# Optimization experiments

Hardware: AMD Instinct MI355X
Metric: run time of the kernel (lower is better)

The kernel has to match this reference:

```python
import jax, jax.numpy as jnp
import numpy as np

B, S, D, H = 4, 1024, 1024, 16
HD = D // H  # head dim = 64


def setup_inputs() -> dict:
    key = jax.random.key(0)
    ks = jax.random.split(key, 12)
    inv = 1.0 / np.sqrt(D)
    inp = {
        "q": jax.random.normal(ks[0], (B, S, D), jnp.float32),
        "k": jax.random.normal(ks[1], (B, S, D), jnp.float32),
        "v": jax.random.normal(ks[2], (B, S, D), jnp.float32),
        # additive-style mask: 1 where attention is disallowed (causal)
        "mask": jnp.triu(jnp.ones((S, S), jnp.float32), k=1)[None, None, :, :],
        "Wq": jax.random.normal(ks[3], (D, D), jnp.float32) * inv,
        "bq": jnp.zeros((D,), jnp.float32),
        "Wk": jax.random.normal(ks[4], (D, D), jnp.float32) * inv,
        "bk": jnp.zeros((D,), jnp.float32),
        "Wv": jax.random.normal(ks[5], (D, D), jnp.float32) * inv,
        "bv": jnp.zeros((D,), jnp.float32),
        "Wo": jax.random.normal(ks[6], (D, D), jnp.float32) * inv,
        "bo": jnp.zeros((D,), jnp.float32),
    }
    return inp


def _split_heads(x):
    # [b, s, (h d)] -> [b, h, s, d]
    b, s, _ = x.shape
    return x.reshape(b, s, H, HD).transpose(0, 2, 1, 3)


def reference(q, k, v, mask, Wq, bq, Wk, bk, Wv, bv, Wo, bo):
    query = _split_heads(q @ Wq + bq)   # [b,h,s,d]
    key = _split_heads(k @ Wk + bk)
    value = _split_heads(v @ Wv + bv)

    scores = jnp.einsum("bhqd,bhkd->bhqk", query, key) / np.sqrt(HD)
    scores = scores + mask * (-1e12)
    attention_weights = jax.nn.softmax(scores, axis=-1)  # [b,h,s,s]
    attn = jnp.einsum("bhqk,bhkd->bhqd", attention_weights, value)

    # dropout is identity in eval mode
    attn = attn.transpose(0, 2, 1, 3).reshape(q.shape[0], q.shape[1], D)
    out = attn @ Wo + bo
    return out, attention_weights
```

## Files before the change

kernel.cpp:

```cpp
#include <hip/hip_runtime.h>
#include <hip/hip_bf16.h>

#define B_ 4
#define S_ 1024
#define D_ 1024
#define H_ 16
#define HD_ 64
#define M_ (B_*S_)
#define NT_ (S_/64)

typedef __attribute__((ext_vector_type(8))) short bf16x8;
typedef __attribute__((ext_vector_type(8))) unsigned short u16x8;
typedef __attribute__((ext_vector_type(4))) float f32x4;

typedef __attribute__((address_space(1))) const unsigned int g_uint;
typedef __attribute__((address_space(3))) unsigned int l_uint;

__device__ __forceinline__ unsigned short f2bf(float f) {
  unsigned int x = __builtin_bit_cast(unsigned int, f);
  unsigned int r = (x + 0x7fffu + ((x >> 16) & 1u)) >> 16;
  return (unsigned short)r;
}
__device__ __forceinline__ float bf2f(unsigned short u) {
  unsigned int x = ((unsigned int)u) << 16;
  return __builtin_bit_cast(float, x);
}
__device__ __forceinline__ void load_lds16(const ushort* g, ushort* l) {
  __builtin_amdgcn_global_load_lds((g_uint*)g, (l_uint*)l, 16, 0, 0);
}

__global__ void cvt3(const float* __restrict__ q, const float* __restrict__ k,
                     const float* __restrict__ v, ushort* __restrict__ qo,
                     ushort* __restrict__ ko, ushort* __restrict__ vo) {
  const float* s; ushort* d;
  switch (blockIdx.y) {
    case 0: s = q; d = qo; break;
    case 1: s = k; d = ko; break;
    default: s = v; d = vo; break;
  }
  int n4 = (M_ * D_) / 4;
  for (int i = blockIdx.x * blockDim.x + threadIdx.x; i < n4; i += gridDim.x * blockDim.x) {
    float4 x = reinterpret_cast<const float4*>(s)[i];
    ushort4 o;
    o.x = f2bf(x.x); o.y = f2bf(x.y); o.z = f2bf(x.z); o.w = f2bf(x.w);
    reinterpret_cast<ushort4*>(d)[i] = o;
  }
}

__global__ void tr4(const float* __restrict__ Wq, const float* __restrict__ Wk,
                    const float* __restrict__ Wv, const float* __restrict__ Wo,
                    ushort* __restrict__ q, ushort* __restrict__ k,
                    ushort* __restrict__ v, ushort* __restrict__ o) {
  const float* W; ushort* WT;
  switch (blockIdx.z) {
    case 0: W = Wq; WT = q; break;
    case 1: W = Wk; WT = k; break;
    case 2: W = Wv; WT = v; break;
    default: W = Wo; WT = o; break;
  }
  __shared__ float tile[32][33];
  int tx = threadIdx.x & 31, ty = threadIdx.x >> 5;
  int bx = blockIdx.x * 32, by = blockIdx.y * 32;
  for (int r = 0; r < 32; r += 8)
    tile[ty + r][tx] = W[(size_t)(by + ty + r) * D_ + bx + tx];
  __syncthreads();
  for (int r = 0; r < 32; r += 8)
    WT[(size_t)(bx + ty + r) * D_ + by + tx] = f2bf(tile[tx][ty + r]);
}

template <int BF16OUT>
__device__ __forceinline__ void gemm_body(const ushort* __restrict__ A,
                                          const ushort* __restrict__ Bt,
                                          const float* __restrict__ bias,
                                          void* __restrict__ Cp,
                                          int bm, int bn, int N, int K) {
  __shared__ ushort Al[128 * 64];
  __shared__ ushort Bl[128 * 64];
  const int tid = threadIdx.x;
  const int wave = tid >> 6, lane = tid & 63;
  const int r0 = lane & 15, kq = lane >> 4;
  const int wr = wave >> 1, wc = wave & 1;
  const int sl = lane >> 3;
  const int sc8 = ((lane & 7) ^ sl) * 8;
  f32x4 zero = {0.f, 0.f, 0.f, 0.f};
  f32x4 acc[4][4];
#pragma unroll
  for (int m = 0; m < 4; ++m)
#pragma unroll
    for (int n = 0; n < 4; ++n) acc[m][n] = zero;

  for (int kt = 0; kt < K; kt += 64) {
    __syncthreads();
#pragma unroll
    for (int i = 0; i < 4; ++i) {
      int c = wave * 4 + i;
      load_lds16(A  + (size_t)(bm + c * 8 + sl) * K + kt + sc8, &Al[c * 512]);
      load_lds16(Bt + (size_t)(bn + c * 8 + sl) * K + kt + sc8, &Bl[c * 512]);
    }
    __syncthreads();
#pragma unroll
    for (int kk = 0; kk < 2; ++kk) {
      bf16x8 a[4], b[4];
#pragma unroll
      for (int m = 0; m < 4; ++m)
        a[m] = *(const bf16x8*)&Al[(wr * 64 + m * 16 + r0) * 64 + (((kk * 4 + kq) ^ (r0 & 7)) * 8)];
#pragma unroll
      for (int n = 0; n < 4; ++n)
        b[n] = *(const bf16x8*)&Bl[(wc * 64 + n * 16 + r0) * 64 + (((kk * 4 + kq) ^ (r0 & 7)) * 8)];
#pragma unroll
      for (int m = 0; m < 4; ++m)
#pragma unroll
        for (int n = 0; n < 4; ++n)
          acc[m][n] = __builtin_amdgcn_mfma_f32_16x16x32_bf16(a[m], b[n], acc[m][n], 0, 0, 0);
    }
  }

#pragma unroll
  for (int m = 0; m < 4; ++m) {
#pragma unroll
    for (int n = 0; n < 4; ++n) {
      int col = bn + wc * 64 + n * 16 + r0;
      float bv = bias[col];
#pragma unroll
      for (int j = 0; j < 4; ++j) {
        int row = bm + wr * 64 + m * 16 + kq * 4 + j;
        float v = acc[m][n][j] + bv;
        if (BF16OUT) ((ushort*)Cp)[(size_t)row * N + col] = f2bf(v);
        else         ((float*)Cp)[(size_t)row * N + col] = v;
      }
    }
  }
}

__global__ __launch_bounds__(256) void gemm_qkv(const ushort* __restrict__ qa,
                                                const ushort* __restrict__ ka,
                                                const ushort* __restrict__ va,
                                                const ushort* __restrict__ WqT,
                                                const ushort* __restrict__ WkT,
                                                const ushort* __restrict__ WvT,
                                                const float* __restrict__ bq,
                                                const float* __restrict__ bk,
                                                const float* __restrict__ bv,
                                                ushort* __restrict__ Qo,
                                                ushort* __restrict__ Ko,
                                                ushort* __restrict__ Vo) {
  const ushort* A; const ushort* Bt; const float* bias; ushort* C;
  switch (blockIdx.z) {
    case 0: A = qa; Bt = WqT; bias = bq; C = Qo; break;
    case 1: A = ka; Bt = WkT; bias = bk; C = Ko; break;
    default: A = va; Bt = WvT; bias = bv; C = Vo; break;
  }
  gemm_body<1>(A, Bt, bias, C, blockIdx.x * 128, blockIdx.y * 128, D_, D_);
}

__global__ __launch_bounds__(256) void gemm_out(const ushort* __restrict__ A,
                                                const ushort* __restrict__ Bt,
                                                const float* __restrict__ bias,
                                                float* __restrict__ C) {
  gemm_body<0>(A, Bt, bias, C, blockIdx.x * 128, blockIdx.y * 128, D_, D_);
}

__global__ __launch_bounds__(256) void attn_fused(const ushort* __restrict__ Qb,
                                                  const ushort* __restrict__ Kb,
                                                  const ushort* __restrict__ Vb,
                                                  float* __restrict__ wout,
                                                  ushort* __restrict__ ctx) {
  const int id = blockIdx.x;
  const int bh = id & 63;
  const int b = bh >> 4, h = bh & 15;
  const int qt = NT_ - 1 - (id >> 6);
  const int tid = threadIdx.x, wave = tid >> 6, lane = tid & 63;
  const int r0 = lane & 15, kq = lane >> 4;
  const int sl = lane >> 3;
  const int sc8 = ((lane & 7) ^ sl) * 8;
  __shared__ ushort Kt[2][64 * 64];
  __shared__ ushort Vt[2][64 * 64];
  __shared__ ushort Wl[4][16 * 64];
  __shared__ float rs_lds[4][16];
  const size_t bh_off = ((size_t)(b * S_)) * D_ + (size_t)h * 64;
  float* wbase = wout + (size_t)bh * S_ * S_;

  const ushort* Qg = Qb + bh_off + (size_t)(qt * 64 + wave * 16 + r0) * D_ + kq * 8;
  bf16x8 qa0 = *(const bf16x8*)Qg;
  bf16x8 qa1 = *(const bf16x8*)(Qg + 32);
  const int grow0 = qt * 64 + wave * 16 + kq * 4;

  auto stage_K = [&](int buf, int vb) {
    const ushort* Kg = Kb + bh_off + (size_t)(vb * 64) * D_;
#pragma unroll
    for (int i = 0; i < 2; ++i) {
      int c = wave * 2 + i;
      load_lds16(Kg + (size_t)(c * 8 + sl) * D_ + sc8, &Kt[buf][c * 512]);
    }
  };

  int cur = 0;
  stage_K(0, 0);
  float partial[4] = {0.f, 0.f, 0.f, 0.f};
  for (int vb = 0; vb <= qt; ++vb) {
    asm volatile("s_waitcnt vmcnt(0)" ::: "memory");
    __builtin_amdgcn_s_barrier();
    if (vb < qt) stage_K(cur ^ 1, vb + 1);
    const bool diag = (vb == qt);
#pragma unroll
    for (int jt = 0; jt < 4; ++jt) {
      int krow = jt * 16 + r0;
      bf16x8 kb0 = *(const bf16x8*)&Kt[cur][krow * 64 + ((kq ^ (r0 & 7)) * 8)];
      bf16x8 kb1 = *(const bf16x8*)&Kt[cur][krow * 64 + (((4 + kq) ^ (r0 & 7)) * 8)];
      f32x4 sc = {0.f, 0.f, 0.f, 0.f};
      sc = __builtin_amdgcn_mfma_f32_16x16x32_bf16(qa0, kb0, sc, 0, 0, 0);
      sc = __builtin_amdgcn_mfma_f32_16x16x32_bf16(qa1, kb1, sc, 0, 0, 0);
      int col = vb * 64 + krow;
#pragma unroll
      for (int j = 0; j < 4; ++j) {
        float e = (diag && col > grow0 + j) ? 0.f : __expf(sc[j] * 0.125f);
        partial[j] += e;
      }
    }
    cur ^= 1;
  }
  float rs[4];
#pragma unroll
  for (int j = 0; j < 4; ++j) {
    float s = partial[j];
#pragma unroll
    for (int off = 1; off < 16; off <<= 1) s += __shfl_xor(s, off, 64);
    rs[j] = 1.f / s;
  }
  if (r0 == 0) {
#pragma unroll
    for (int j = 0; j < 4; ++j) rs_lds[wave][kq * 4 + j] = rs[j];
  }

  f32x4 zero = {0.f, 0.f, 0.f, 0.f};
  f32x4 cacc[4];
#pragma unroll
  for (int nt = 0; nt < 4; ++nt) cacc[nt] = zero;

  __syncthreads();
  const int row16 = lane >> 2, c4 = lane & 3;
  const float sclw = rs_lds[wave][row16];
  uint4 vr[2];
  auto vload = [&](int vb) {
    const ushort* Vg = Vb + bh_off + (size_t)(vb * 64) * D_;
    vr[0] = *(const uint4*)&Vg[(size_t)lane * D_ + (size_t)(wave * 2 + 0) * 8];
    vr[1] = *(const uint4*)&Vg[(size_t)lane * D_ + (size_t)(wave * 2 + 1) * 8];
  };
  auto vwrite = [&](int buf) {
#pragma unroll
    for (int it = 0; it < 2; ++it) {
      int seg = wave * 2 + it;
      ushort tmp[8];
      *(uint4*)tmp = vr[it];
#pragma unroll
      for (int e = 0; e < 8; ++e) Vt[buf][(seg * 8 + e) * 64 + (lane ^ (e << 3))] = tmp[e];
    }
  };
  cur = 0;
  stage_K(0, 0);
  vload(0);
  vwrite(0);
  for (int vb = 0; vb <= qt; ++vb) {
    if (vb == 0) asm volatile("s_waitcnt vmcnt(0) lgkmcnt(0)" ::: "memory");
    else         asm volatile("s_waitcnt vmcnt(4) lgkmcnt(0)" ::: "memory");
    __builtin_amdgcn_s_barrier();
    if (vb < qt) { stage_K(cur ^ 1, vb + 1); vload(vb + 1); }
    const bool diag = (vb == qt);
#pragma unroll
    for (int jt = 0; jt < 4; ++jt) {
      int krow = jt * 16 + r0;
      bf16x8 kb0 = *(const bf16x8*)&Kt[cur][krow * 64 + ((kq ^ (r0 & 7)) * 8)];
      bf16x8 kb1 = *(const bf16x8*)&Kt[cur][krow * 64 + (((4 + kq) ^ (r0 & 7)) * 8)];
      f32x4 sc = {0.f, 0.f, 0.f, 0.f};
      sc = __builtin_amdgcn_mfma_f32_16x16x32_bf16(qa0, kb0, sc, 0, 0, 0);
      sc = __builtin_amdgcn_mfma_f32_16x16x32_bf16(qa1, kb1, sc, 0, 0, 0);
      int col = vb * 64 + krow;
#pragma unroll
      for (int j = 0; j < 4; ++j) {
        int rowW = kq * 4 + j;
        float e = (diag && col > grow0 + j) ? 0.f : __expf(sc[j] * 0.125f);
        Wl[wave][rowW * 64 + ((jt * 16 + r0) ^ ((rowW & 7) << 3))] = f2bf(e);
      }
    }
#pragma unroll
    for (int ks = 0; ks < 2; ++ks) {
      bf16x8 af = *(const bf16x8*)&Wl[wave][r0 * 64 + (((ks * 4 + kq) ^ (r0 & 7)) * 8)];
#pragma unroll
      for (int nt = 0; nt < 4; ++nt) {
        bf16x8 vf = *(const bf16x8*)&Vt[cur][(nt * 16 + r0) * 64 + (((ks * 4 + kq) ^ (r0 & 7)) * 8)];
        cacc[nt] = __builtin_amdgcn_mfma_f32_16x16x32_bf16(af, vf, cacc[nt], 0, 0, 0);
      }
    }
    {
      int slotA = (2 * c4) ^ (row16 & 7);
      int slotB = (2 * c4 + 1) ^ (row16 & 7);
      u16x8 w0 = *(const u16x8*)&Wl[wave][row16 * 64 + slotA * 8];
      u16x8 w1 = *(const u16x8*)&Wl[wave][row16 * 64 + slotB * 8];
      float* dst = &wbase[(size_t)(qt * 64 + wave * 16 + row16) * S_ + vb * 64 + c4 * 16];
      f32x4 o0 = {bf2f(w0[0]) * sclw, bf2f(w0[1]) * sclw, bf2f(w0[2]) * sclw, bf2f(w0[3]) * sclw};
      f32x4 o1 = {bf2f(w0[4]) * sclw, bf2f(w0[5]) * sclw, bf2f(w0[6]) * sclw, bf2f(w0[7]) * sclw};
      f32x4 o2 = {bf2f(w1[0]) * sclw, bf2f(w1[1]) * sclw, bf2f(w1[2]) * sclw, bf2f(w1[3]) * sclw};
      f32x4 o3 = {bf2f(w1[4]) * sclw, bf2f(w1[5]) * sclw, bf2f(w1[6]) * sclw, bf2f(w1[7]) * sclw};
      *(f32x4*)&dst[0]  = o0;
      *(f32x4*)&dst[4]  = o1;
      *(f32x4*)&dst[8]  = o2;
      *(f32x4*)&dst[12] = o3;
    }
    if (vb < qt) vwrite(cur ^ 1);
    cur ^= 1;
  }

  {
    int col0 = (qt + 1) * 64;
    int nf4 = (S_ - col0) >> 2;
    int row = tid >> 2, c = tid & 3;
    f32x4 z4 = {0.f, 0.f, 0.f, 0.f};
    float* rp = &wbase[(size_t)(qt * 64 + row) * S_];
    for (int i = c; i < nf4; i += 4) *(f32x4*)&rp[col0 + i * 4] = z4;
  }

  {
    ushort* cg = ctx + ((size_t)(b * S_ + qt * 64 + wave * 16 + kq * 4)) * D_ + h * 64;
#pragma unroll
    for (int nt = 0; nt < 4; ++nt)
#pragma unroll
      for (int j = 0; j < 4; ++j)
        cg[(size_t)j * D_ + nt * 16 + r0] = f2bf(cacc[nt][j] * rs[j]);
  }
}

extern "C" void kernel_launch(void* const* d_in, const int* in_sizes, int n_in,
                              void* d_out, int out_size, void* d_ws, size_t ws_size,
                              hipStream_t stream) {
  const float* q    = (const float*)d_in[0];
  const float* k    = (const float*)d_in[1];
  const float* v    = (const float*)d_in[2];
  const float* Wq   = (const float*)d_in[4];
  const float* bq   = (const float*)d_in[5];
  const float* Wk   = (const float*)d_in[6];
  const float* bk   = (const float*)d_in[7];
  const float* Wv   = (const float*)d_in[8];
  const float* bv   = (const float*)d_in[9];
  const float* Wo   = (const float*)d_in[10];
  const float* bo   = (const float*)d_in[11];

  char* ws = (char*)d_ws;
  const size_t MB = 1024 * 1024;
  ushort* q_bf   = (ushort*)(ws + 0 * MB);
  ushort* k_bf   = (ushort*)(ws + 8 * MB);
  ushort* v_bf   = (ushort*)(ws + 16 * MB);
  ushort* WqT    = (ushort*)(ws + 24 * MB);
  ushort* WkT    = (ushort*)(ws + 26 * MB);
  ushort* WvT    = (ushort*)(ws + 28 * MB);
  ushort* WoT    = (ushort*)(ws + 30 * MB);
  ushort* Q_bf   = (ushort*)(ws + 32 * MB);
  ushort* K_bf   = (ushort*)(ws + 40 * MB);
  ushort* V_bf   = (ushort*)(ws + 48 * MB);
  ushort* ctx_bf = (ushort*)(ws + 56 * MB);

  float* out  = (float*)d_out;
  float* wout = out + (size_t)M_ * D_;

  cvt3<<<dim3(2048, 3), 256, 0, stream>>>(q, k, v, q_bf, k_bf, v_bf);
  tr4<<<dim3(32, 32, 4), 256, 0, stream>>>(Wq, Wk, Wv, Wo, WqT, WkT, WvT, WoT);
  gemm_qkv<<<dim3(M_ / 128, D_ / 128, 3), 256, 0, stream>>>(
      q_bf, k_bf, v_bf, WqT, WkT, WvT, bq, bk, bv, Q_bf, K_bf, V_bf);
  attn_fused<<<dim3(1024), 256, 0, stream>>>(Q_bf, K_bf, V_bf, wout, ctx_bf);
  gemm_out<<<dim3(M_ / 128, D_ / 128), 256, 0, stream>>>(ctx_bf, WoT, bo, out);
}
```

Baseline: 169.5 us.

## Transpose QK^T MFMA so lanes own query rows and write weights directly

Swaps the MFMA operands so each lane holds four consecutive key columns for a single query row. Row sums then need only two cross-lane shuffles, and the normalized fp32 attention weights can be stored straight from registers as float4. This drops the LDS round-trip and the bf16-to-fp32 reconversion that the weight output path used before. It also replaces __expf with exp2f using a pre-folded log2e scale and packs the bf16 conversions with v_cvt_pk_bf16_f32 under a new LDS swizzle. In exchange, the global weight stores become 16-byte per-lane writes scattered across 16 rows, which may coalesce worse than the previous 64-byte row segments.

```diff
diff --git a/kernel.cpp b/kernel.cpp
--- a/kernel.cpp
+++ b/kernel.cpp
@@ -24,6 +24,11 @@
 __device__ __forceinline__ float bf2f(unsigned short u) {
   unsigned int x = ((unsigned int)u) << 16;
   return __builtin_bit_cast(float, x);
+}
+__device__ __forceinline__ unsigned int cvtpk(float lo, float hi) {
+  unsigned int r;
+  asm("v_cvt_pk_bf16_f32 %0, %1, %2" : "=v"(r) : "v"(lo), "v"(hi));
+  return r;
 }
 __device__ __forceinline__ void load_lds16(const ushort* g, ushort* l) {
   __builtin_amdgcn_global_load_lds((g_uint*)g, (l_uint*)l, 16, 0, 0);
@@ -176,14 +181,14 @@
   __shared__ ushort Kt[2][64 * 64];
   __shared__ ushort Vt[2][64 * 64];
   __shared__ ushort Wl[4][16 * 64];
-  __shared__ float rs_lds[4][16];
   const size_t bh_off = ((size_t)(b * S_)) * D_ + (size_t)h * 64;
   float* wbase = wout + (size_t)bh * S_ * S_;
+  const float KSC = 0.18033688011f;
 
   const ushort* Qg = Qb + bh_off + (size_t)(qt * 64 + wave * 16 + r0) * D_ + kq * 8;
   bf16x8 qa0 = *(const bf16x8*)Qg;
   bf16x8 qa1 = *(const bf16x8*)(Qg + 32);
-  const int grow0 = qt * 64 + wave * 16 + kq * 4;
+  const int qglob = qt * 64 + wave * 16 + r0;
 
   auto stage_K = [&](int buf, int vb) {
     const ushort* Kg = Kb + bh_off + (size_t)(vb * 64) * D_;
@@ -196,7 +201,7 @@
 
   int cur = 0;
   stage_K(0, 0);
-  float partial[4] = {0.f, 0.f, 0.f, 0.f};
+  float p0 = 0.f, p1 = 0.f, p2 = 0.f, p3 = 0.f;
   for (int vb = 0; vb <= qt; ++vb) {
     asm volatile("s_waitcnt vmcnt(0)" ::: "memory");
     __builtin_amdgcn_s_barrier();
@@ -208,29 +213,20 @@
       bf16x8 kb0 = *(const bf16x8*)&Kt[cur][krow * 64 + ((kq ^ (r0 & 7)) * 8)];
       bf16x8 kb1 = *(const bf16x8*)&Kt[cur][krow * 64 + (((4 + kq) ^ (r0 & 7)) * 8)];
       f32x4 sc = {0.f, 0.f, 0.f, 0.f};
-      sc = __builtin_amdgcn_mfma_f32_16x16x32_bf16(qa0, kb0, sc, 0, 0, 0);
-      sc = __builtin_amdgcn_mfma_f32_16x16x32_bf16(qa1, kb1, sc, 0, 0, 0);
-      int col = vb * 64 + krow;
-#pragma unroll
-      for (int j = 0; j < 4; ++j) {
-        float e = (diag && col > grow0 + j) ? 0.f : __expf(sc[j] * 0.125f);
-        partial[j] += e;
-      }
+      sc = __builtin_amdgcn_mfma_f32_16x16x32_bf16(kb0, qa0, sc, 0, 0, 0);
+      sc = __builtin_amdgcn_mfma_f32_16x16x32_bf16(kb1, qa1, sc, 0, 0, 0);
+      int k0 = vb * 64 + jt * 16 + kq * 4;
+      p0 += (diag && k0 + 0 > qglob) ? 0.f : exp2f(sc[0] * KSC);
+      p1 += (diag && k0 + 1 > qglob) ? 0.f : exp2f(sc[1] * KSC);
+      p2 += (diag && k0 + 2 > qglob) ? 0.f : exp2f(sc[2] * KSC);
+      p3 += (diag && k0 + 3 > qglob) ? 0.f : exp2f(sc[3] * KSC);
     }
     cur ^= 1;
   }
-  float rs[4];
-#pragma unroll
-  for (int j = 0; j < 4; ++j) {
-    float s = partial[j];
-#pragma unroll
-    for (int off = 1; off < 16; off <<= 1) s += __shfl_xor(s, off, 64);
-    rs[j] = 1.f / s;
-  }
-  if (r0 == 0) {
-#pragma unroll
-    for (int j = 0; j < 4; ++j) rs_lds[wave][kq * 4 + j] = rs[j];
-  }
+  float ssum = (p0 + p1) + (p2 + p3);
+  ssum += __shfl_xor(ssum, 16, 64);
+  ssum += __shfl_xor(ssum, 32, 64);
+  const float rs = 1.f / ssum;
 
   f32x4 zero = {0.f, 0.f, 0.f, 0.f};
   f32x4 cacc[4];
@@ -238,8 +234,6 @@
   for (int nt = 0; nt < 4; ++nt) cacc[nt] = zero;
 
   __syncthreads();
-  const int row16 = lane >> 2, c4 = lane & 3;
-  const float sclw = rs_lds[wave][row16];
   uint4 vr[2];
   auto vload = [&](int vb) {
     const ushort* Vg = Vb + bh_off + (size_t)(vb * 64) * D_;
@@ -272,39 +266,30 @@
       bf16x8 kb0 = *(const bf16x8*)&Kt[cur][krow * 64 + ((kq ^ (r0 & 7)) * 8)];
       bf16x8 kb1 = *(const bf16x8*)&Kt[cur][krow * 64 + (((4 + kq) ^ (r0 & 7)) * 8)];
       f32x4 sc = {0.f, 0.f, 0.f, 0.f};
-      sc = __builtin_amdgcn_mfma_f32_16x16x32_bf16(qa0, kb0, sc, 0, 0, 0);
-      sc = __builtin_amdgcn_mfma_f32_16x16x32_bf16(qa1, kb1, sc, 0, 0, 0);
-      int col = vb * 64 + krow;
-#pragma unroll
-      for (int j = 0; j < 4; ++j) {
-        int rowW = kq * 4 + j;
-        float e = (diag && col > grow0 + j) ? 0.f : __expf(sc[j] * 0.125f);
-        Wl[wave][rowW * 64 + ((jt * 16 + r0) ^ ((rowW & 7) << 3))] = f2bf(e);
-      }
+      sc = __builtin_amdgcn_mfma_f32_16x16x32_bf16(kb0, qa0, sc, 0, 0, 0);
+      sc = __builtin_amdgcn_mfma_f32_16x16x32_bf16(kb1, qa1, sc, 0, 0, 0);
+      int k0 = vb * 64 + jt * 16 + kq * 4;
+      float e0 = (diag && k0 + 0 > qglob) ? 0.f : exp2f(sc[0] * KSC);
+      float e1 = (diag && k0 + 1 > qglob) ? 0.f : exp2f(sc[1] * KSC);
+      float e2 = (diag && k0 + 2 > qglob) ? 0.f : exp2f(sc[2] * KSC);
+      float e3 = (diag && k0 + 3 > qglob) ? 0.f : exp2f(sc[3] * KSC);
+      uint2 pk;
+      pk.x = cvtpk(e0, e1);
+      pk.y = cvtpk(e2, e3);
+      int s = (4 * jt + kq) ^ ((r0 & 3) << 2);
+      *(uint2*)&Wl[wave][r0 * 64 + s * 4] = pk;
+      f32x4 o = {e0 * rs, e1 * rs, e2 * rs, e3 * rs};
+      *(f32x4*)&wbase[(size_t)qglob * S_ + k0] = o;
     }
 #pragma unroll
     for (int ks = 0; ks < 2; ++ks) {
-      bf16x8 af = *(const bf16x8*)&Wl[wave][r0 * 64 + (((ks * 4 + kq) ^ (r0 & 7)) * 8)];
+      int sB = (8 * ks + 2 * kq) ^ ((r0 & 3) << 2);
+      bf16x8 af = *(const bf16x8*)&Wl[wave][r0 * 64 + sB * 4];
 #pragma unroll
       for (int nt = 0; nt < 4; ++nt) {
         bf16x8 vf = *(const bf16x8*)&Vt[cur][(nt * 16 + r0) * 64 + (((ks * 4 + kq) ^ (r0 & 7)) * 8)];
         cacc[nt] = __builtin_amdgcn_mfma_f32_16x16x32_bf16(af, vf, cacc[nt], 0, 0, 0);
       }
-    }
-    {
-      int slotA = (2 * c4) ^ (row16 & 7);
-      int slotB = (2 * c4 + 1) ^ (row16 & 7);
-      u16x8 w0 = *(const u16x8*)&Wl[wave][row16 * 64 + slotA * 8];
-      u16x8 w1 = *(const u16x8*)&Wl[wave][row16 * 64 + slotB * 8];
-      float* dst = &wbase[(size_t)(qt * 64 + wave * 16 + row16) * S_ + vb * 64 + c4 * 16];
-      f32x4 o0 = {bf2f(w0[0]) * sclw, bf2f(w0[1]) * sclw, bf2f(w0[2]) * sclw, bf2f(w0[3]) * sclw};
-      f32x4 o1 = {bf2f(w0[4]) * sclw, bf2f(w0[5]) * sclw, bf2f(w0[6]) * sclw, bf2f(w0[7]) * sclw};
-      f32x4 o2 = {bf2f(w1[0]) * sclw, bf2f(w1[1]) * sclw, bf2f(w1[2]) * sclw, bf2f(w1[3]) * sclw};
-      f32x4 o3 = {bf2f(w1[4]) * sclw, bf2f(w1[5]) * sclw, bf2f(w1[6]) * sclw, bf2f(w1[7]) * sclw};
-      *(f32x4*)&dst[0]  = o0;
-      *(f32x4*)&dst[4]  = o1;
-      *(f32x4*)&dst[8]  = o2;
-      *(f32x4*)&dst[12] = o3;
     }
     if (vb < qt) vwrite(cur ^ 1);
     cur ^= 1;
@@ -320,12 +305,15 @@
   }
 
   {
+    float rsj[4];
+#pragma unroll
+    for (int j = 0; j < 4; ++j) rsj[j] = __shfl(rs, kq * 4 + j, 64);
     ushort* cg = ctx + ((size_t)(b * S_ + qt * 64 + wave * 16 + kq * 4)) * D_ + h * 64;
 #pragma unroll
     for (int nt = 0; nt < 4; ++nt)
 #pragma unroll
       for (int j = 0; j < 4; ++j)
-        cg[(size_t)j * D_ + nt * 16 + r0] = f2bf(cacc[nt][j] * rs[j]);
+        cg[(size_t)j * D_ + nt * 16 + r0] = f2bf(cacc[nt][j] * rsj[j]);
   }
 }
 
```

Result: no change. 171.6 us, median of 3 (+1.2%).
